# Performance work log

Measured on AMD Instinct MI355X. Metric: run time of the kernel, lower is better.

## Reference

```python
import jax, jax.numpy as jnp
import numpy as np

D_MODEL = 1024
NUM_HEADS = 16
HEAD_DIM = D_MODEL // NUM_HEADS
FF_HIDDEN = 2 * D_MODEL
EPS = 1e-5


def _layernorm(x, g, b):
    mu = jnp.mean(x, axis=-1, keepdims=True)
    var = jnp.var(x, axis=-1, keepdims=True)
    return (x - mu) * jax.lax.rsqrt(var + EPS) * g + b


def setup_inputs() -> dict:
    key = jax.random.key(0)
    ks = jax.random.split(key, 12)
    s = lambda fan_in: 1.0 / np.sqrt(fan_in)
    return {
        "x": jax.random.normal(ks[0], (4, 2048, D_MODEL), dtype=jnp.float32),
        "qkv_w": jax.random.uniform(ks[1], (D_MODEL, 3 * D_MODEL), minval=-s(D_MODEL), maxval=s(D_MODEL)),
        "qkv_b": jax.random.uniform(ks[2], (3 * D_MODEL,), minval=-s(D_MODEL), maxval=s(D_MODEL)),
        "out_w": jax.random.uniform(ks[3], (D_MODEL, D_MODEL), minval=-s(D_MODEL), maxval=s(D_MODEL)),
        "out_b": jax.random.uniform(ks[4], (D_MODEL,), minval=-s(D_MODEL), maxval=s(D_MODEL)),
        "ff1_w": jax.random.uniform(ks[5], (D_MODEL, FF_HIDDEN), minval=-s(D_MODEL), maxval=s(D_MODEL)),
        "ff1_b": jax.random.uniform(ks[6], (FF_HIDDEN,), minval=-s(D_MODEL), maxval=s(D_MODEL)),
        "ff2_w": jax.random.uniform(ks[7], (FF_HIDDEN, D_MODEL), minval=-s(FF_HIDDEN), maxval=s(FF_HIDDEN)),
        "ff2_b": jax.random.uniform(ks[8], (D_MODEL,), minval=-s(FF_HIDDEN), maxval=s(FF_HIDDEN)),
        "ln1_g": jnp.ones((D_MODEL,), jnp.float32),
        "ln1_b": jnp.zeros((D_MODEL,), jnp.float32),
        "ln2_g": jnp.ones((D_MODEL,), jnp.float32),
        "ln2_b": jnp.zeros((D_MODEL,), jnp.float32),
    }


def reference(x, qkv_w, qkv_b, out_w, out_b, ff1_w, ff1_b, ff2_w, ff2_b, ln1_g, ln1_b, ln2_g, ln2_b):
    B, L, _ = x.shape
    scale = HEAD_DIM ** -0.5
    # pre-norm attention
    h = _layernorm(x, ln1_g, ln1_b)
    qkv = h @ qkv_w + qkv_b  # [B,L,3D]
    q, k, v = jnp.split(qkv, 3, axis=-1)
    reshape = lambda t: t.reshape(B, L, NUM_HEADS, HEAD_DIM).transpose(0, 2, 1, 3)  # [B,H,L,Dh]
    q, k, v = reshape(q), reshape(k), reshape(v)
    attn = jnp.einsum('bhqd,bhkd->bhqk', q, k) * scale  # [B,H,L,L]
    attn = jax.nn.softmax(attn, axis=-1)
    ctx = jnp.einsum('bhqk,bhkd->bhqd', attn, v)
    ctx = ctx.transpose(0, 2, 1, 3).reshape(B, L, D_MODEL)
    attended = ctx @ out_w + out_b
    x = x + attended
    # pre-norm FFN with exact GELU (torch default)
    h2 = _layernorm(x, ln2_g, ln2_b)
    ff = jax.nn.gelu(h2 @ ff1_w + ff1_b, approximate=False) @ ff2_w + ff2_b
    return x + ff
```

## Files before the change

### kernel.cpp

```cpp
#include <hip/hip_runtime.h>

#define AS1 __attribute__((address_space(1)))
#define AS3 __attribute__((address_space(3)))

typedef unsigned short u16;
typedef __bf16 bf16x8 __attribute__((ext_vector_type(8)));
typedef float floatx4 __attribute__((ext_vector_type(4)));
typedef float floatx16 __attribute__((ext_vector_type(16)));
typedef u16 u16x8 __attribute__((ext_vector_type(8)));
typedef u16 u16x4 __attribute__((ext_vector_type(4)));
typedef unsigned uintx4 __attribute__((ext_vector_type(4)));

__device__ __forceinline__ float bf2f(u16 u) { return __uint_as_float(((unsigned)u) << 16); }
__device__ __forceinline__ u16 f2bf(float f) {
    unsigned u = __float_as_uint(f);
    u += 0x7FFFu + ((u >> 16) & 1u);
    return (u16)(u >> 16);
}
__device__ __forceinline__ unsigned packbf2(float f0, float f1) {
    return __builtin_amdgcn_perm(__float_as_uint(f1), __float_as_uint(f0), 0x07060302u);
}
__device__ __forceinline__ void gl_lds16(const u16* g, u16* l) {
    __builtin_amdgcn_global_load_lds((const AS1 void*)g, (AS3 void*)l, 16, 0, 0);
}

__global__ __launch_bounds__(256) void transpose_all(const float* __restrict__ w0, u16* __restrict__ o0,
                                                     const float* __restrict__ w1, u16* __restrict__ o1,
                                                     const float* __restrict__ w2, u16* __restrict__ o2,
                                                     const float* __restrict__ w3, u16* __restrict__ o3) {
    __shared__ u16 t[32][33];
    int blk = blockIdx.x;
    const float* in;
    u16* out;
    int R, C, bx, by;
    if (blk < 3072) {
        in = w0; out = o0; R = 1024; C = 3072; bx = blk % 96; by = blk / 96;
    } else if (blk < 4096) {
        blk -= 3072; in = w1; out = o1; R = 1024; C = 1024; bx = blk % 32; by = blk / 32;
    } else if (blk < 6144) {
        blk -= 4096; in = w2; out = o2; R = 1024; C = 2048; bx = blk % 64; by = blk / 64;
    } else {
        blk -= 6144; in = w3; out = o3; R = 2048; C = 1024; bx = blk % 32; by = blk / 32;
    }
    const int c0 = bx * 32, r0 = by * 32;
    const int tx = threadIdx.x, ty = threadIdx.y;
#pragma unroll
    for (int i = 0; i < 4; i++)
        t[ty + i * 8][tx] = f2bf(in[(size_t)(r0 + ty + i * 8) * C + c0 + tx]);
    __syncthreads();
#pragma unroll
    for (int i = 0; i < 4; i++) out[(size_t)(c0 + ty + i * 8) * R + r0 + tx] = t[tx][ty + i * 8];
}

__global__ __launch_bounds__(256) void ln_k(const float* __restrict__ x, const float* __restrict__ g,
                                            const float* __restrict__ b, u16* __restrict__ out) {
    const int row = blockIdx.x, tid = threadIdx.x;
    const float4 xv = *(const float4*)(x + (size_t)row * 1024 + tid * 4);
    float f[4] = {xv.x, xv.y, xv.z, xv.w};
    float s1 = 0.f, s2 = 0.f;
#pragma unroll
    for (int e = 0; e < 4; e++) {
        s1 += f[e];
        s2 += f[e] * f[e];
    }
#pragma unroll
    for (int off = 32; off >= 1; off >>= 1) {
        s1 += __shfl_down(s1, off);
        s2 += __shfl_down(s2, off);
    }
    __shared__ float w1[4], w2[4];
    const int wave = tid >> 6, lane = tid & 63;
    if (lane == 0) { w1[wave] = s1; w2[wave] = s2; }
    __syncthreads();
    s1 = w1[0] + w1[1] + w1[2] + w1[3];
    s2 = w2[0] + w2[1] + w2[2] + w2[3];
    const float mu = s1 * (1.0f / 1024.0f);
    const float var = s2 * (1.0f / 1024.0f) - mu * mu;
    const float rs = rsqrtf(var + 1e-5f);
    const float4 gv = *(const float4*)(g + tid * 4);
    const float4 bv = *(const float4*)(b + tid * 4);
    const float gf[4] = {gv.x, gv.y, gv.z, gv.w}, bff[4] = {bv.x, bv.y, bv.z, bv.w};
    u16x4 o;
#pragma unroll
    for (int e = 0; e < 4; e++) o[e] = f2bf((f[e] - mu) * rs * gf[e] + bff[e]);
    *(u16x4*)(out + (size_t)row * 1024 + tid * 4) = o;
}

template <int GELU, int RESID, int F32OUT, int KSWZ>
__global__ __launch_bounds__(256, 4) void gemm_bt(const u16* __restrict__ A, const u16* __restrict__ Bt,
                                                  const float* __restrict__ bias,
                                                  const float* __restrict__ resid, void* __restrict__ Cv,
                                                  int M, int N, int K, int lda) {
    __shared__ u16 Al[2][128 * 32];
    __shared__ u16 Bl[2][128 * 32];
    const int tid = threadIdx.x;
    const int wave = tid >> 6, lane = tid & 63;
    const int g16 = lane >> 4, l16 = lane & 15;
    const int m0 = blockIdx.y * 128, n0 = blockIdx.x * 128;
    const int wm = (wave >> 1) * 64, wn = (wave & 1) * 64;
    const int csw = (l16 >> 1) & 3;

    floatx4 acc[4][4] = {};

    const int scs = ((lane & 3) ^ ((lane >> 3) & 3)) * 8;
    const u16* Ag = A + (size_t)(m0 + (lane >> 2)) * lda + scs;
    const u16* Bg = Bt + (size_t)(n0 + (lane >> 2)) * K + scs;

    auto stage = [&](int buf, int k0) {
#pragma unroll
        for (int i = 0; i < 2; i++) {
            const int ro = 16 * (wave * 2 + i);
            gl_lds16(Ag + (size_t)ro * lda + k0, &Al[buf][(wave * 2 + i) * 512]);
            gl_lds16(Bg + (size_t)ro * K + k0, &Bl[buf][(wave * 2 + i) * 512]);
        }
    };

    stage(0, 0);
    __syncthreads();
    int buf = 0;
    for (int k0 = 0; k0 < K; k0 += 32) {
        if (k0 + 32 < K) stage(buf ^ 1, k0 + 32);
        bf16x8 af[4], bfr[4];
#pragma unroll
        for (int i = 0; i < 4; i++)
            af[i] = *(const bf16x8*)&Al[buf][(wm + i * 16 + l16) * 32 + ((g16 ^ csw) << 3)];
#pragma unroll
        for (int j = 0; j < 4; j++)
            bfr[j] = *(const bf16x8*)&Bl[buf][(wn + j * 16 + l16) * 32 + ((g16 ^ csw) << 3)];
#pragma unroll
        for (int i = 0; i < 4; i++)
#pragma unroll
            for (int j = 0; j < 4; j++)
                acc[i][j] = __builtin_amdgcn_mfma_f32_16x16x32_bf16(af[i], bfr[j], acc[i][j], 0, 0, 0);
        __syncthreads();
        buf ^= 1;
    }

    float bv[4];
#pragma unroll
    for (int j = 0; j < 4; j++) bv[j] = bias[n0 + wn + j * 16 + l16];
#pragma unroll
    for (int i = 0; i < 4; i++) {
#pragma unroll
        for (int r = 0; r < 4; r++) {
            const int gm = m0 + wm + i * 16 + g16 * 4 + r;
            const size_t ro = (size_t)gm * N;
#pragma unroll
            for (int j = 0; j < 4; j++) {
                int gn = n0 + wn + j * 16 + l16;
                float v = acc[i][j][r] + bv[j];
                if (GELU) v = 0.5f * v * (1.0f + erff(v * 0.70710678118654752f));
                if (RESID) v += resid[ro + gn];
                if (KSWZ && ((gn >> 10) == 1)) gn ^= (gm & 7) << 3;
                if (F32OUT)
                    ((float*)Cv)[ro + gn] = v;
                else
                    ((u16*)Cv)[ro + gn] = f2bf(v);
            }
        }
    }
}

__global__ __launch_bounds__(256) void attn_prep(const u16* __restrict__ qkv, u16* __restrict__ Vsw) {
    __shared__ u16 Tl[64][72];
    const int bh = blockIdx.y, b = bh >> 4, h = bh & 15;
    const int kt = blockIdx.x * 64;
    const int t = threadIdx.x;
    const size_t qbase = (size_t)b * 2048 * 3072;
    const int r = t >> 2, cpi = (t & 3) * 2;

    const u16* vrow = qkv + qbase + (size_t)(kt + r) * 3072 + 2048 + h * 64;
    *(u16x8*)&Tl[r][cpi * 8] = *(const u16x8*)(vrow + cpi * 8);
    *(u16x8*)&Tl[r][(cpi + 1) * 8] = *(const u16x8*)(vrow + (cpi + 1) * 8);
    __syncthreads();
    {
        const int d = r;
        u16* dst = Vsw + ((size_t)bh * 64 + d) * 2048 + kt;
#pragma unroll
        for (int i = 0; i < 2; i++) {
            const int cp = cpi + i;
            const int c = cp ^ (d & 7);
            u16x8 tmp;
#pragma unroll
            for (int e = 0; e < 8; e++) tmp[e] = Tl[c * 8 + e][d];
            *(u16x8*)(dst + cp * 8) = tmp;
        }
    }
}

__global__ __launch_bounds__(256, 4) void attn_k(u16* __restrict__ qkv, const u16* __restrict__ Vsw) {
    __shared__ u16 Kl[2][64 * 64];
    __shared__ u16 Vt[2][64 * 64];
    const int tid = threadIdx.x;
    const int w = tid >> 6, lane = tid & 63;
    const int l31 = lane & 31, half = lane >> 5, swz = lane & 7;
    const int bh = blockIdx.y, b = bh >> 4, h = bh & 15;
    const int q0 = blockIdx.x * 128 + w * 32;
    const size_t qbase = (size_t)b * 2048 * 3072;
    const size_t vbase = (size_t)bh * 64 * 2048;

    bf16x8 bq[4];
    {
        const u16* qp = qkv + qbase + (size_t)(q0 + l31) * 3072 + h * 64;
        const float sc = 0.125f * 1.44269504088896340736f;
#pragma unroll
        for (int kd = 0; kd < 4; kd++) {
            const u16x8 raw = *(const u16x8*)(qp + kd * 16 + half * 8);
            u16 tmp[8];
#pragma unroll
            for (int e = 0; e < 8; e++) tmp[e] = f2bf(bf2f(raw[e]) * sc);
            bq[kd] = *(const bf16x8*)tmp;
        }
    }

    floatx16 accO[2] = {};
    float lsum = 0.f;

    auto stage = [&](int buf, int kt) {
#pragma unroll
        for (int i = 0; i < 2; i++) {
            const int rr = w * 16 + i * 8 + (lane >> 3);
            gl_lds16(qkv + qbase + (size_t)(kt + rr) * 3072 + 1024 + h * 64 + (lane & 7) * 8,
                     &Kl[buf][(w * 16 + i * 8) * 64]);
            gl_lds16(Vsw + vbase + (size_t)rr * 2048 + kt + (lane & 7) * 8,
                     &Vt[buf][(w * 16 + i * 8) * 64]);
        }
    };

    stage(0, 0);
    __syncthreads();
    int buf = 0;
    for (int kt = 0; kt < 2048; kt += 64) {
        if (kt + 64 < 2048) stage(buf ^ 1, kt + 64);

        floatx16 accS[2] = {};
#pragma unroll
        for (int kb = 0; kb < 2; kb++)
#pragma unroll
            for (int kd = 0; kd < 4; kd++) {
                const bf16x8 ak =
                    *(const bf16x8*)&Kl[buf][(kb * 32 + l31) * 64 + ((kd * 2 + half) ^ swz) * 8];
                accS[kb] = __builtin_amdgcn_mfma_f32_32x32x16_bf16(ak, bq[kd], accS[kb], 0, 0, 0);
            }

        uintx4 Pf[4];
#pragma unroll
        for (int kb = 0; kb < 2; kb++) {
            float E[16];
#pragma unroll
            for (int e = 0; e < 16; e++) {
                E[e] = exp2f(accS[kb][e]);
                lsum += E[e];
            }
#pragma unroll
            for (int kp = 0; kp < 2; kp++) {
                unsigned x0 = packbf2(E[8 * kp + 0], E[8 * kp + 1]);
                unsigned x1 = packbf2(E[8 * kp + 2], E[8 * kp + 3]);
                unsigned y0 = packbf2(E[8 * kp + 4], E[8 * kp + 5]);
                unsigned y1 = packbf2(E[8 * kp + 6], E[8 * kp + 7]);
                asm volatile("v_permlane32_swap_b32 %0, %1" : "+v"(x0), "+v"(y0));
                asm volatile("v_permlane32_swap_b32 %0, %1" : "+v"(x1), "+v"(y1));
                uintx4 f;
                f[0] = x0; f[1] = x1; f[2] = y0; f[3] = y1;
                Pf[kb * 2 + kp] = f;
            }
        }

#pragma unroll
        for (int kd = 0; kd < 4; kd++) {
            const bf16x8 bp = __builtin_bit_cast(bf16x8, Pf[kd]);
#pragma unroll
            for (int db = 0; db < 2; db++) {
                const bf16x8 av =
                    *(const bf16x8*)&Vt[buf][(db * 32 + l31) * 64 + ((kd * 2 + half) ^ swz) * 8];
                accO[db] = __builtin_amdgcn_mfma_f32_32x32x16_bf16(av, bp, accO[db], 0, 0, 0);
            }
        }
        __syncthreads();
        buf ^= 1;
    }

    lsum += __shfl_xor(lsum, 32);
    const float rinv = 1.0f / lsum;
    u16* cw = qkv + qbase + (size_t)(q0 + l31) * 3072 + 2048 + h * 64;
#pragma unroll
    for (int db = 0; db < 2; db++)
#pragma unroll
        for (int rg = 0; rg < 4; rg++) {
            const int d0 = db * 32 + 8 * rg + 4 * half;
            u16x4 o;
#pragma unroll
            for (int rr2 = 0; rr2 < 4; rr2++) o[rr2] = f2bf(accO[db][rg * 4 + rr2] * rinv);
            *(u16x4*)(cw + d0) = o;
        }
}

extern "C" void kernel_launch(void* const* d_in, const int* in_sizes, int n_in, void* d_out,
                              int out_size, void* d_ws, size_t ws_size, hipStream_t stream) {
    const float* x = (const float*)d_in[0];
    const float* qkv_w = (const float*)d_in[1];
    const float* qkv_b = (const float*)d_in[2];
    const float* out_w = (const float*)d_in[3];
    const float* out_b = (const float*)d_in[4];
    const float* ff1_w = (const float*)d_in[5];
    const float* ff1_b = (const float*)d_in[6];
    const float* ff2_w = (const float*)d_in[7];
    const float* ff2_b = (const float*)d_in[8];
    const float* ln1_g = (const float*)d_in[9];
    const float* ln1_b = (const float*)d_in[10];
    const float* ln2_g = (const float*)d_in[11];
    const float* ln2_b = (const float*)d_in[12];
    float* out = (float*)d_out;

    char* ws = (char*)d_ws;
    u16* qkvT = (u16*)(ws);
    u16* outT = (u16*)(ws + 6291456);
    u16* ff1T = (u16*)(ws + 8388608);
    u16* ff2T = (u16*)(ws + 12582912);
    u16* hbuf = (u16*)(ws + 16777216);
    u16* big  = (u16*)(ws + 33554432);

    transpose_all<<<8192, dim3(32, 8), 0, stream>>>(qkv_w, qkvT, out_w, outT, ff1_w, ff1T, ff2_w, ff2T);

    ln_k<<<8192, 256, 0, stream>>>(x, ln1_g, ln1_b, hbuf);
    gemm_bt<0, 0, 0, 1><<<dim3(24, 64), 256, 0, stream>>>(hbuf, qkvT, qkv_b, nullptr, big, 8192, 3072, 1024, 1024);
    attn_prep<<<dim3(32, 64), 256, 0, stream>>>(big, hbuf);
    attn_k<<<dim3(16, 64), 256, 0, stream>>>(big, hbuf);
    gemm_bt<0, 1, 1, 0><<<dim3(8, 64), 256, 0, stream>>>(big + 2048, outT, out_b, x, out, 8192, 1024, 1024, 3072);
    ln_k<<<8192, 256, 0, stream>>>(out, ln2_g, ln2_b, hbuf);
    gemm_bt<1, 0, 0, 0><<<dim3(16, 64), 256, 0, stream>>>(hbuf, ff1T, ff1_b, nullptr, big, 8192, 2048, 1024, 1024);
    gemm_bt<0, 1, 1, 0><<<dim3(8, 64), 256, 0, stream>>>(big, ff2T, ff2_b, out, out, 8192, 1024, 2048, 2048);
}
```

Baseline: 463.7 us.

## Software-pipeline attention loop: compute next QK tile after PV with priority hints

The flash-attention inner loop is split into qk, softmax_pack and pv stages. The loop is reordered so the QK^T MFMAs for the next key tile are issued right after the barrier, and the exp/pack softmax work of one tile can overlap matrix work in other waves. s_setprio raises wave priority around the MFMA blocks, and the row sum is split into four partial accumulators to shorten the dependent add chain. This costs extra registers to keep the next tile's scores live across iterations, which could lower occupancy.

After: 457.3 us. Within noise of the previous version (-1.4%).

```diff
diff --git a/kernel.cpp b/kernel.cpp
--- a/kernel.cpp
+++ b/kernel.cpp
@@ -214,7 +214,7 @@
     }
 
     floatx16 accO[2] = {};
-    float lsum = 0.f;
+    float lsp[4] = {0.f, 0.f, 0.f, 0.f};
 
     auto stage = [&](int buf, int kt) {
 #pragma unroll
@@ -227,30 +227,28 @@
         }
     };
 
-    stage(0, 0);
-    __syncthreads();
-    int buf = 0;
-    for (int kt = 0; kt < 2048; kt += 64) {
-        if (kt + 64 < 2048) stage(buf ^ 1, kt + 64);
-
-        floatx16 accS[2] = {};
+    auto qk = [&](int bufi, floatx16* S) {
+        floatx16 t[2] = {};
 #pragma unroll
         for (int kb = 0; kb < 2; kb++)
 #pragma unroll
             for (int kd = 0; kd < 4; kd++) {
                 const bf16x8 ak =
-                    *(const bf16x8*)&Kl[buf][(kb * 32 + l31) * 64 + ((kd * 2 + half) ^ swz) * 8];
-                accS[kb] = __builtin_amdgcn_mfma_f32_32x32x16_bf16(ak, bq[kd], accS[kb], 0, 0, 0);
-            }
-
-        uintx4 Pf[4];
+                    *(const bf16x8*)&Kl[bufi][(kb * 32 + l31) * 64 + ((kd * 2 + half) ^ swz) * 8];
+                t[kb] = __builtin_amdgcn_mfma_f32_32x32x16_bf16(ak, bq[kd], t[kb], 0, 0, 0);
+            }
+        S[0] = t[0];
+        S[1] = t[1];
+    };
+
+    auto softmax_pack = [&](const floatx16* S, uintx4* Pf) {
 #pragma unroll
         for (int kb = 0; kb < 2; kb++) {
             float E[16];
 #pragma unroll
             for (int e = 0; e < 16; e++) {
-                E[e] = exp2f(accS[kb][e]);
-                lsum += E[e];
+                E[e] = exp2f(S[kb][e]);
+                lsp[e & 3] += E[e];
             }
 #pragma unroll
             for (int kp = 0; kp < 2; kp++) {
@@ -265,21 +263,48 @@
                 Pf[kb * 2 + kp] = f;
             }
         }
-
+    };
+
+    auto pv = [&](int bufi, const uintx4* Pf) {
 #pragma unroll
         for (int kd = 0; kd < 4; kd++) {
             const bf16x8 bp = __builtin_bit_cast(bf16x8, Pf[kd]);
 #pragma unroll
             for (int db = 0; db < 2; db++) {
                 const bf16x8 av =
-                    *(const bf16x8*)&Vt[buf][(db * 32 + l31) * 64 + ((kd * 2 + half) ^ swz) * 8];
+                    *(const bf16x8*)&Vt[bufi][(db * 32 + l31) * 64 + ((kd * 2 + half) ^ swz) * 8];
                 accO[db] = __builtin_amdgcn_mfma_f32_32x32x16_bf16(av, bp, accO[db], 0, 0, 0);
             }
         }
+    };
+
+    stage(0, 0);
+    __syncthreads();
+    stage(1, 64);
+    floatx16 accS[2];
+    qk(0, accS);
+
+    int buf = 0;
+    for (int kt = 0; kt < 2048 - 64; kt += 64) {
+        uintx4 Pf[4];
+        softmax_pack(accS, Pf);
+        __builtin_amdgcn_s_setprio(1);
+        pv(buf, Pf);
+        __builtin_amdgcn_s_setprio(0);
         __syncthreads();
+        if (kt + 128 < 2048) stage(buf, kt + 128);
+        __builtin_amdgcn_s_setprio(1);
+        qk(buf ^ 1, accS);
+        __builtin_amdgcn_s_setprio(0);
         buf ^= 1;
     }
-
+    {
+        uintx4 Pf[4];
+        softmax_pack(accS, Pf);
+        pv(buf, Pf);
+    }
+
+    float lsum = (lsp[0] + lsp[1]) + (lsp[2] + lsp[3]);
     lsum += __shfl_xor(lsum, 32);
     const float rinv = 1.0f / lsum;
     u16* cw = qkv + qbase + (size_t)(q0 + l31) * 3072 + 2048 + h * 64;
```
